# Optimization experiments

Hardware: AMD Instinct MI355X
Metric: run time of the kernel (lower is better)

Reference implementation:

```python
import jax, jax.numpy as jnp
import numpy as np

N_USERS = 100000
N_ITEMS = 100000
N = N_USERS + N_ITEMS
E = 3200000
TXT = 768
GREC = 16
D = 32            # embedding_dim (hardcoded 32 in the torch module)
LAYERS = 3        # len(weight_size)


def setup_inputs() -> dict:
    key = jax.random.key(0)
    ks = jax.random.split(key, 20)
    inp = {}
    inp["edge_row"] = jax.random.randint(ks[0], (E,), 0, N, dtype=jnp.int32)
    inp["edge_col"] = jax.random.randint(ks[1], (E,), 0, N, dtype=jnp.int32)
    # normalized adjacency values (positive, small)
    inp["adj_vals"] = jax.random.uniform(ks[2], (E,), dtype=jnp.float32) * 0.1
    inp["user_name_embs"] = jax.random.normal(ks[3], (N_USERS, TXT), dtype=jnp.float32)
    inp["sent_embs"] = jax.random.normal(ks[4], (N_ITEMS, TXT), dtype=jnp.float32)
    # learned params
    inp["user_emb"] = jax.random.normal(ks[5], (N_USERS, GREC), dtype=jnp.float32) * 0.1
    inp["item_emb"] = jax.random.normal(ks[6], (N_ITEMS, GREC), dtype=jnp.float32) * 0.1
    inp["ue_W1"] = jax.random.normal(ks[7], (TXT, 32), dtype=jnp.float32) * 0.05
    inp["ue_W2"] = jax.random.normal(ks[8], (32, GREC), dtype=jnp.float32) * 0.05
    inp["ie_W1"] = jax.random.normal(ks[9], (TXT, 32), dtype=jnp.float32) * 0.05
    inp["ie_W2"] = jax.random.normal(ks[10], (32, GREC), dtype=jnp.float32) * 0.05
    inp["gc_W"] = jax.random.normal(ks[11], (LAYERS, D, D), dtype=jnp.float32) * 0.1
    inp["gc_b"] = jnp.zeros((LAYERS, D), dtype=jnp.float32)
    inp["bi_W"] = jax.random.normal(ks[12], (LAYERS, D, D), dtype=jnp.float32) * 0.1
    inp["bi_b"] = jnp.zeros((LAYERS, D), dtype=jnp.float32)
    return inp


def _ngcf_forward(edge_row, edge_col, adj_vals, user_name_embs, sent_embs,
                  user_emb, item_emb, ue_W1, ue_W2, ie_W1, ie_W2,
                  gc_W, gc_b, bi_W, bi_b):
    # text encoders (Dropout is identity in eval mode)
    u_created = jax.nn.relu(user_name_embs @ ue_W1) @ ue_W2   # [Nu, 16]
    i_created = jax.nn.relu(sent_embs @ ie_W1) @ ie_W2         # [Ni, 16]
    agg_user = jnp.concatenate([user_emb, u_created], axis=1)  # [Nu, 32]
    agg_item = jnp.concatenate([item_emb, i_created], axis=1)  # [Ni, 32]
    ego = jnp.concatenate([agg_user, agg_item], axis=0)        # [N, 32]

    all_embeddings = [ego]
    for l in range(LAYERS):
        # sparse.mm(adj, ego): gather source rows, scale by edge value, scatter-add
        gathered = adj_vals[:, None] * ego[edge_col]           # [E, 32]
        side = jax.ops.segment_sum(gathered, edge_row, num_segments=N)  # [N, 32]
        sum_emb = jax.nn.leaky_relu(side @ gc_W[l] + gc_b[l])
        bi_emb = jax.nn.leaky_relu((ego * side) @ bi_W[l] + bi_b[l])
        ego = sum_emb + bi_emb                                 # dropout = identity (eval)
        norm = ego / jnp.maximum(
            jnp.linalg.norm(ego, axis=1, keepdims=True), 1e-12)
        all_embeddings.append(norm)
    return jnp.concatenate(all_embeddings, axis=1)             # [N, 32*(LAYERS+1)]


def reference(edge_row, edge_col, adj_vals, user_name_embs, sent_embs,
              user_emb, item_emb, ue_W1, ue_W2, ie_W1, ie_W2,
              gc_W, gc_b, bi_W, bi_b):
    all_e = _ngcf_forward(edge_row, edge_col, adj_vals, user_name_embs, sent_embs,
                          user_emb, item_emb, ue_W1, ue_W2, ie_W1, ie_W2,
                          gc_W, gc_b, bi_W, bi_b)
    u_g = all_e[:N_USERS]
    i_g = all_e[N_USERS:]
    return (u_g, i_g)
```

## Files before the change

### kernel.cpp

```cpp
#include <hip/hip_runtime.h>
#include <cstdint>

#define NU 100000
#define NI 100000
#define NN 200000
#define NE 3200000
#define TXT 768
#define DD 32
#define NRANGE 8
#define ROWS_PER_RANGE (NN / NRANGE)
#define NBJ 313

typedef _Float16 f16x8 __attribute__((ext_vector_type(8)));
typedef _Float16 f16x4 __attribute__((ext_vector_type(4)));
typedef float    f32x4 __attribute__((ext_vector_type(4)));

__device__ __forceinline__ float lrelu(float x) { return x >= 0.f ? x : 0.01f * x; }

__global__ void copy_emb_kernel(const float* __restrict__ uemb,
                                const float* __restrict__ iemb,
                                _Float16* __restrict__ ego16,
                                float* __restrict__ outp)
{
    int idx = blockIdx.x * blockDim.x + threadIdx.x;
    if (idx >= NN * 4) return;
    int n = idx >> 2, q = idx & 3;
    float4 v;
    if (n < NU) v = ((const float4*)uemb)[(size_t)n * 4 + q];
    else        v = ((const float4*)iemb)[(size_t)(n - NU) * 4 + q];
    f16x4 h;
    h[0] = (_Float16)v.x; h[1] = (_Float16)v.y;
    h[2] = (_Float16)v.z; h[3] = (_Float16)v.w;
    *(f16x4*)(ego16 + (size_t)n * 32 + q * 4) = h;
    ((float4*)outp)[(size_t)n * 32 + q] = v;
}

__global__ __launch_bounds__(256) void pack_w1_kernel(const float* __restrict__ ueW1,
                                                      const float* __restrict__ ieW1,
                                                      _Float16* __restrict__ w1p)
{
    const int i    = blockIdx.x * 256 + threadIdx.x;
    const int side = blockIdx.y;
    const float* W1 = side ? ieW1 : ueW1;
    int j   = i & 7;
    int ln  = (i >> 3) & 63;
    int kbH = i >> 9;
    int kb  = kbH >> 1, H = kbH & 1;
    int k   = kb * 32 + (ln >> 4) * 8 + j;
    int c   = H * 16 + (ln & 15);
    w1p[side * 24576 + i] = (_Float16)W1[k * 32 + c];
}

__global__ __launch_bounds__(512, 8) void mlp_mfma_kernel(
    const float* __restrict__ Xu, const float* __restrict__ Xi,
    const _Float16* __restrict__ w1pack,
    const float* __restrict__ ueW2, const float* __restrict__ ieW2,
    _Float16* __restrict__ ego16,
    float* __restrict__ outp)
{
    __shared__ _Float16 hbuf[8][640];

    const int tid  = threadIdx.x;
    const int lane = tid & 63;
    const int wv   = tid >> 6;

    const bool isU = blockIdx.x < 512;
    const float* X  = isU ? Xu : Xi;
    const _Float16* w1p = w1pack + (isU ? 0 : 24576);
    const float* W2 = isU ? ueW2 : ieW2;
    const int node_base = isU ? 0 : NU;
    const int bj = isU ? blockIdx.x : blockIdx.x - 512;

    f16x8 bw2;
    #pragma unroll
    for (int j = 0; j < 8; ++j)
        bw2[j] = (_Float16)W2[((lane >> 4) * 8 + j) * 16 + (lane & 15)];

    _Float16* hb = &hbuf[wv][0];
    const int gw = bj * 8 + wv;
    const int t0 = (int)(((long)gw * 6250) >> 12);
    const int t1 = (int)(((long)(gw + 1) * 6250) >> 12);

    for (int tile = t0; tile < t1; ++tile) {
        const float* xp = X + (size_t)(tile * 16 + (lane & 15)) * TXT + (lane >> 4) * 8;
        f32x4 c0 = {0.f, 0.f, 0.f, 0.f};
        f32x4 c1 = {0.f, 0.f, 0.f, 0.f};

        #pragma unroll 4
        for (int kb = 0; kb < 24; ++kb) {
            float4 xa = *(const float4*)(xp + kb * 32);
            float4 xb = *(const float4*)(xp + kb * 32 + 4);
            f16x8 b0 = *(const f16x8*)&w1p[(kb * 2 + 0) * 512 + lane * 8];
            f16x8 b1 = *(const f16x8*)&w1p[(kb * 2 + 1) * 512 + lane * 8];
            f16x8 a;
            a[0] = (_Float16)xa.x; a[1] = (_Float16)xa.y;
            a[2] = (_Float16)xa.z; a[3] = (_Float16)xa.w;
            a[4] = (_Float16)xb.x; a[5] = (_Float16)xb.y;
            a[6] = (_Float16)xb.z; a[7] = (_Float16)xb.w;
            c0 = __builtin_amdgcn_mfma_f32_16x16x32_f16(a, b0, c0, 0, 0, 0);
            c1 = __builtin_amdgcn_mfma_f32_16x16x32_f16(a, b1, c1, 0, 0, 0);
        }

        #pragma unroll
        for (int j = 0; j < 4; ++j) {
            int r = (lane >> 4) * 4 + j;
            hb[r * 40 + (lane & 15)]      = (_Float16)fmaxf(c0[j], 0.f);
            hb[r * 40 + (lane & 15) + 16] = (_Float16)fmaxf(c1[j], 0.f);
        }
        const _Float16* ap = &hb[(lane & 15) * 40 + (lane >> 4) * 8];
        f16x4 lo = *(const f16x4*)ap;
        f16x4 hi = *(const f16x4*)(ap + 4);
        f16x8 a2;
        a2[0] = lo[0]; a2[1] = lo[1]; a2[2] = lo[2]; a2[3] = lo[3];
        a2[4] = hi[0]; a2[5] = hi[1]; a2[6] = hi[2]; a2[7] = hi[3];

        f32x4 c2 = {0.f, 0.f, 0.f, 0.f};
        c2 = __builtin_amdgcn_mfma_f32_16x16x32_f16(a2, bw2, c2, 0, 0, 0);

        const int rbase = node_base + tile * 16 + (lane >> 4) * 4;
        const int j2 = lane & 15;
        #pragma unroll
        for (int j = 0; j < 4; ++j) {
            float v = c2[j];
            ego16[(size_t)(rbase + j) * 32  + 16 + j2] = (_Float16)v;
            outp [(size_t)(rbase + j) * 128 + 16 + j2] = v;
        }
    }
}

__global__ __launch_bounds__(256) void count_ranged_kernel(const int* __restrict__ erow,
                                                           int* __restrict__ cnt)
{
    const int rlo = (blockIdx.x & 7) * ROWS_PER_RANGE;
    const int rhi = rlo + ROWS_PER_RANGE;
    const int bj  = blockIdx.x >> 3;
    const int4* e4 = (const int4*)erow;
    for (int c = bj * 256 + threadIdx.x; c < NE / 4; c += NBJ * 256) {
        int4 v = e4[c];
        if (v.x >= rlo && v.x < rhi) atomicAdd(&cnt[v.x], 1);
        if (v.y >= rlo && v.y < rhi) atomicAdd(&cnt[v.y], 1);
        if (v.z >= rlo && v.z < rhi) atomicAdd(&cnt[v.z], 1);
        if (v.w >= rlo && v.w < rhi) atomicAdd(&cnt[v.w], 1);
    }
}

__global__ __launch_bounds__(256) void scan_blk_kernel(const int* __restrict__ cnt,
                                                       int* __restrict__ rp,
                                                       int* __restrict__ bsum)
{
    __shared__ int ts[256];
    const int tid = threadIdx.x;
    const int base = blockIdx.x * 1024 + tid * 4;
    int v0 = (base + 0 < NN) ? cnt[base + 0] : 0;
    int v1 = (base + 1 < NN) ? cnt[base + 1] : 0;
    int v2 = (base + 2 < NN) ? cnt[base + 2] : 0;
    int v3 = (base + 3 < NN) ? cnt[base + 3] : 0;
    int s = v0 + v1 + v2 + v3;
    ts[tid] = s;
    __syncthreads();
    for (int off = 1; off < 256; off <<= 1) {
        int t = (tid >= off) ? ts[tid - off] : 0;
        __syncthreads();
        ts[tid] += t;
        __syncthreads();
    }
    int excl = ts[tid] - s;
    if (base + 0 < NN) rp[base + 0] = excl;
    if (base + 1 < NN) rp[base + 1] = excl + v0;
    if (base + 2 < NN) rp[base + 2] = excl + v0 + v1;
    if (base + 3 < NN) rp[base + 3] = excl + v0 + v1 + v2;
    if (tid == 255) bsum[blockIdx.x] = ts[255];
}

__global__ __launch_bounds__(256) void scan_bsum_kernel(int* __restrict__ bsum, int nblk)
{
    __shared__ int ts[256];
    const int tid = threadIdx.x;
    int v = (tid < nblk) ? bsum[tid] : 0;
    ts[tid] = v;
    __syncthreads();
    for (int off = 1; off < 256; off <<= 1) {
        int t = (tid >= off) ? ts[tid - off] : 0;
        __syncthreads();
        ts[tid] += t;
        __syncthreads();
    }
    if (tid < nblk) bsum[tid] = ts[tid] - v;
}

__global__ __launch_bounds__(256) void add_off_kernel(int* __restrict__ rp,
                                                      const int* __restrict__ bsum,
                                                      int* __restrict__ cur)
{
    int i = blockIdx.x * 256 + threadIdx.x;
    if (i < NN) {
        int v = rp[i] + bsum[i >> 10];
        rp[i] = v;
        cur[i] = v;
    }
    if (i == 0) rp[NN] = NE;
}

__global__ __launch_bounds__(256) void fill_ranged_kernel(const int* __restrict__ erow,
                                                          const int* __restrict__ ecol,
                                                          const float* __restrict__ eval,
                                                          int* __restrict__ cur,
                                                          uint2* __restrict__ recs)
{
    const int rlo = (blockIdx.x & 7) * ROWS_PER_RANGE;
    const int rhi = rlo + ROWS_PER_RANGE;
    const int bj  = blockIdx.x >> 3;
    const int4* e4 = (const int4*)erow;
    for (int c = bj * 256 + threadIdx.x; c < NE / 4; c += NBJ * 256) {
        int4 v = e4[c];
        int base = c * 4;
        if (v.x >= rlo && v.x < rhi) {
            int pos = atomicAdd(&cur[v.x], 1);
            recs[pos] = make_uint2((unsigned)ecol[base+0] | ((unsigned)(v.x & 63) << 18),
                                   __float_as_uint(eval[base+0]));
        }
        if (v.y >= rlo && v.y < rhi) {
            int pos = atomicAdd(&cur[v.y], 1);
            recs[pos] = make_uint2((unsigned)ecol[base+1] | ((unsigned)(v.y & 63) << 18),
                                   __float_as_uint(eval[base+1]));
        }
        if (v.z >= rlo && v.z < rhi) {
            int pos = atomicAdd(&cur[v.z], 1);
            recs[pos] = make_uint2((unsigned)ecol[base+2] | ((unsigned)(v.z & 63) << 18),
                                   __float_as_uint(eval[base+2]));
        }
        if (v.w >= rlo && v.w < rhi) {
            int pos = atomicAdd(&cur[v.w], 1);
            recs[pos] = make_uint2((unsigned)ecol[base+3] | ((unsigned)(v.w & 63) << 18),
                                   __float_as_uint(eval[base+3]));
        }
    }
}

__global__ __launch_bounds__(256) void pull_update_v2(
    const int* __restrict__ rp, const uint2* __restrict__ recs,
    const _Float16* __restrict__ egoIn, _Float16* __restrict__ egoOut,
    float* __restrict__ outp,
    const float* __restrict__ gcW, const float* __restrict__ gcb,
    const float* __restrict__ biW, const float* __restrict__ bib, int l)
{
    __shared__ float acc[64][33];
    __shared__ float Wg[32][36];
    __shared__ float Wb[32][36];
    __shared__ float bgs[32], bbs[32];

    const int tid = threadIdx.x;
    for (int i = tid; i < 64 * 33; i += 256) ((float*)acc)[i] = 0.f;
    for (int i = tid; i < 1024; i += 256) {
        Wg[i >> 5][i & 31] = gcW[l * 1024 + i];
        Wb[i >> 5][i & 31] = biW[l * 1024 + i];
    }
    if (tid < 32) { bgs[tid] = gcb[l * 32 + tid]; bbs[tid] = bib[l * 32 + tid]; }

    const int r0 = blockIdx.x * 64;
    const int eBeg = rp[r0], eEnd = rp[r0 + 64];
    __syncthreads();

    const int cnt = eEnd - eBeg;
    const int s   = tid >> 3;
    const int q   = tid & 7;
    const int L   = (cnt + 31) >> 5;
    const int e0  = eBeg + s * L;
    const int e1  = min(e0 + L, eEnd);

    float4 a4 = make_float4(0.f, 0.f, 0.f, 0.f);
    int curRl = -1;
    for (int e = e0; e < e1; ++e) {
        uint2 rec = recs[e];
        int col = rec.x & 0x3FFFF;
        int rl  = rec.x >> 18;
        float a = __uint_as_float(rec.y);
        f16x4 v = *(const f16x4*)(egoIn + (size_t)col * 32 + q * 4);
        if (rl != curRl) {
            if (curRl >= 0) {
                atomicAdd(&acc[curRl][q * 4 + 0], a4.x);
                atomicAdd(&acc[curRl][q * 4 + 1], a4.y);
                atomicAdd(&acc[curRl][q * 4 + 2], a4.z);
                atomicAdd(&acc[curRl][q * 4 + 3], a4.w);
            }
            a4 = make_float4(0.f, 0.f, 0.f, 0.f);
            curRl = rl;
        }
        a4.x += a * (float)v[0];
        a4.y += a * (float)v[1];
        a4.z += a * (float)v[2];
        a4.w += a * (float)v[3];
    }
    if (curRl >= 0) {
        atomicAdd(&acc[curRl][q * 4 + 0], a4.x);
        atomicAdd(&acc[curRl][q * 4 + 1], a4.y);
        atomicAdd(&acc[curRl][q * 4 + 2], a4.z);
        atomicAdd(&acc[curRl][q * 4 + 3], a4.w);
    }
    __syncthreads();

    const int r    = tid >> 2;
    const int c    = tid & 3;
    const int node = r0 + r;
    const int j0   = c * 8;

    const _Float16* er = egoIn + (size_t)node * 32;
    f16x8 ev0 = *(const f16x8*)er;
    f16x8 ev1 = *(const f16x8*)(er + 8);
    f16x8 ev2 = *(const f16x8*)(er + 16);
    f16x8 ev3 = *(const f16x8*)(er + 24);

    float A[8], B[8];
    #pragma unroll
    for (int jj = 0; jj < 8; ++jj) { A[jj] = bgs[j0 + jj]; B[jj] = bbs[j0 + jj]; }

    #pragma unroll
    for (int kq = 0; kq < 4; ++kq) {
        #pragma unroll
        for (int kk = 0; kk < 8; ++kk) {
            const int k = kq * 8 + kk;
            float sk = acc[r][k];
            float evk = (kq == 0) ? (float)ev0[kk] : (kq == 1) ? (float)ev1[kk]
                      : (kq == 2) ? (float)ev2[kk] : (float)ev3[kk];
            float ek = sk * evk;
            f32x4 g0 = *(const f32x4*)&Wg[k][j0];
            f32x4 g1 = *(const f32x4*)&Wg[k][j0 + 4];
            f32x4 b0 = *(const f32x4*)&Wb[k][j0];
            f32x4 b1 = *(const f32x4*)&Wb[k][j0 + 4];
            A[0] += sk * g0[0]; A[1] += sk * g0[1]; A[2] += sk * g0[2]; A[3] += sk * g0[3];
            A[4] += sk * g1[0]; A[5] += sk * g1[1]; A[6] += sk * g1[2]; A[7] += sk * g1[3];
            B[0] += ek * b0[0]; B[1] += ek * b0[1]; B[2] += ek * b0[2]; B[3] += ek * b0[3];
            B[4] += ek * b1[0]; B[5] += ek * b1[1]; B[6] += ek * b1[2]; B[7] += ek * b1[3];
        }
    }

    float v[8];
    float ss = 0.f;
    #pragma unroll
    for (int jj = 0; jj < 8; ++jj) {
        float x = lrelu(A[jj]) + lrelu(B[jj]);
        v[jj] = x;
        ss += x * x;
    }
    ss += __shfl_xor(ss, 1, 64);
    ss += __shfl_xor(ss, 2, 64);
    float inv = 1.0f / fmaxf(sqrtf(ss), 1e-12f);

    f16x8 h;
    #pragma unroll
    for (int jj = 0; jj < 8; ++jj) h[jj] = (_Float16)v[jj];
    *(f16x8*)(egoOut + (size_t)node * 32 + j0) = h;

    float* op = outp + (size_t)node * 128 + (size_t)(l + 1) * 32 + j0;
    float4 o0 = make_float4(v[0] * inv, v[1] * inv, v[2] * inv, v[3] * inv);
    float4 o1 = make_float4(v[4] * inv, v[5] * inv, v[6] * inv, v[7] * inv);
    *(float4*)op       = o0;
    *(float4*)(op + 4) = o1;
}

extern "C" void kernel_launch(void* const* d_in, const int* in_sizes, int n_in,
                              void* d_out, int out_size, void* d_ws, size_t ws_size,
                              hipStream_t stream)
{
    const int*   erow = (const int*)d_in[0];
    const int*   ecol = (const int*)d_in[1];
    const float* evalp = (const float*)d_in[2];
    const float* une  = (const float*)d_in[3];
    const float* se   = (const float*)d_in[4];
    const float* uemb = (const float*)d_in[5];
    const float* iemb = (const float*)d_in[6];
    const float* ueW1 = (const float*)d_in[7];
    const float* ueW2 = (const float*)d_in[8];
    const float* ieW1 = (const float*)d_in[9];
    const float* ieW2 = (const float*)d_in[10];
    const float* gcW  = (const float*)d_in[11];
    const float* gcb  = (const float*)d_in[12];
    const float* biW  = (const float*)d_in[13];
    const float* bib  = (const float*)d_in[14];
    float* outp = (float*)d_out;

    _Float16* egoA16 = (_Float16*)d_ws;
    _Float16* egoB16 = egoA16 + (size_t)NN * 32;
    uint2* recs = (uint2*)(egoB16 + (size_t)NN * 32);
    int*   cnt  = (int*)(recs + (size_t)NE);
    int*   rp   = cnt + NN;
    int*   cur  = rp + NN + 1;
    int*   bsum = cur + NN;
    _Float16* w1pack = (_Float16*)(bsum + 256);

    const size_t need = (size_t)((char*)(w1pack + 49152) - (char*)d_ws);
    if (ws_size < need) return;

    pack_w1_kernel<<<dim3(96, 2), 256, 0, stream>>>(ueW1, ieW1, w1pack);
    copy_emb_kernel<<<(NN * 4 + 255) / 256, 256, 0, stream>>>(uemb, iemb, egoA16, outp);
    mlp_mfma_kernel<<<1024, 512, 0, stream>>>(une, se, w1pack, ueW2, ieW2,
                                              egoA16, outp);

    const int NBLK = (NN + 1023) / 1024;
    hipMemsetAsync(cnt, 0, (size_t)NN * sizeof(int), stream);
    count_ranged_kernel<<<NRANGE * NBJ, 256, 0, stream>>>(erow, cnt);
    scan_blk_kernel<<<NBLK, 256, 0, stream>>>(cnt, rp, bsum);
    scan_bsum_kernel<<<1, 256, 0, stream>>>(bsum, NBLK);
    add_off_kernel<<<(NN + 255) / 256, 256, 0, stream>>>(rp, bsum, cur);
    fill_ranged_kernel<<<NRANGE * NBJ, 256, 0, stream>>>(erow, ecol, evalp, cur, recs);

    const _Float16* egoIn = egoA16;
    _Float16* egoOut = egoB16;
    for (int l = 0; l < 3; ++l) {
        pull_update_v2<<<NN / 64, 256, 0, stream>>>(rp, recs, egoIn, egoOut, outp,
                                                    gcW, gcb, biW, bib, l);
        const _Float16* t = egoOut; egoOut = (_Float16*)egoIn; egoIn = t;
    }
}
```

Measured before the change: 790.2 us.

## Merge prep kernels, stage MLP inputs via async LDS loads, unroll gather loop

Folds edge counting, embedding copy and W1 packing into one prep kernel to cut launch count and let the independent work run concurrently. The text-encoder MFMA kernel now double-buffers input tiles in shared memory through direct global-to-LDS loads with a swizzled layout, instead of per-lane strided global loads. Its occupancy hint drops to 4 blocks and it uses 64KB of LDS. The pull kernel issues four gathers at a time so more memory loads are in flight. Risks include lower occupancy and fragile hand-written waitcnt ordering.

Result: faster. 739.2 us (-6.5%).

```diff
diff --git a/kernel.cpp b/kernel.cpp
--- a/kernel.cpp
+++ b/kernel.cpp
@@ -15,50 +15,69 @@
 typedef _Float16 f16x4 __attribute__((ext_vector_type(4)));
 typedef float    f32x4 __attribute__((ext_vector_type(4)));
 
+typedef __attribute__((address_space(1))) const unsigned int guint;
+typedef __attribute__((address_space(3))) unsigned int luint;
+
 __device__ __forceinline__ float lrelu(float x) { return x >= 0.f ? x : 0.01f * x; }
 
-__global__ void copy_emb_kernel(const float* __restrict__ uemb,
-                                const float* __restrict__ iemb,
-                                _Float16* __restrict__ ego16,
-                                float* __restrict__ outp)
-{
-    int idx = blockIdx.x * blockDim.x + threadIdx.x;
-    if (idx >= NN * 4) return;
-    int n = idx >> 2, q = idx & 3;
-    float4 v;
-    if (n < NU) v = ((const float4*)uemb)[(size_t)n * 4 + q];
-    else        v = ((const float4*)iemb)[(size_t)(n - NU) * 4 + q];
-    f16x4 h;
-    h[0] = (_Float16)v.x; h[1] = (_Float16)v.y;
-    h[2] = (_Float16)v.z; h[3] = (_Float16)v.w;
-    *(f16x4*)(ego16 + (size_t)n * 32 + q * 4) = h;
-    ((float4*)outp)[(size_t)n * 32 + q] = v;
-}
-
-__global__ __launch_bounds__(256) void pack_w1_kernel(const float* __restrict__ ueW1,
-                                                      const float* __restrict__ ieW1,
-                                                      _Float16* __restrict__ w1p)
-{
-    const int i    = blockIdx.x * 256 + threadIdx.x;
-    const int side = blockIdx.y;
-    const float* W1 = side ? ieW1 : ueW1;
-    int j   = i & 7;
-    int ln  = (i >> 3) & 63;
-    int kbH = i >> 9;
-    int kb  = kbH >> 1, H = kbH & 1;
-    int k   = kb * 32 + (ln >> 4) * 8 + j;
-    int c   = H * 16 + (ln & 15);
-    w1p[side * 24576 + i] = (_Float16)W1[k * 32 + c];
-}
-
-__global__ __launch_bounds__(512, 8) void mlp_mfma_kernel(
+__global__ __launch_bounds__(256) void prep_kernel(
+    const int* __restrict__ erow,
+    const float* __restrict__ uemb, const float* __restrict__ iemb,
+    const float* __restrict__ ueW1, const float* __restrict__ ieW1,
+    int* __restrict__ cnt,
+    _Float16* __restrict__ ego16, float* __restrict__ outp,
+    _Float16* __restrict__ w1p)
+{
+    const int b = blockIdx.x;
+    const int tid = threadIdx.x;
+
+    if (b < 2504) {
+        const int rlo = (b & 7) * ROWS_PER_RANGE;
+        const int rhi = rlo + ROWS_PER_RANGE;
+        const int bj  = b >> 3;
+        const int4* e4 = (const int4*)erow;
+        for (int c = bj * 256 + tid; c < NE / 4; c += NBJ * 256) {
+            int4 v = e4[c];
+            if (v.x >= rlo && v.x < rhi) atomicAdd(&cnt[v.x], 1);
+            if (v.y >= rlo && v.y < rhi) atomicAdd(&cnt[v.y], 1);
+            if (v.z >= rlo && v.z < rhi) atomicAdd(&cnt[v.z], 1);
+            if (v.w >= rlo && v.w < rhi) atomicAdd(&cnt[v.w], 1);
+        }
+    } else if (b < 2504 + 3125) {
+        int idx = (b - 2504) * 256 + tid;
+        if (idx >= NN * 4) return;
+        int n = idx >> 2, q = idx & 3;
+        float4 v;
+        if (n < NU) v = ((const float4*)uemb)[(size_t)n * 4 + q];
+        else        v = ((const float4*)iemb)[(size_t)(n - NU) * 4 + q];
+        f16x4 h;
+        h[0] = (_Float16)v.x; h[1] = (_Float16)v.y;
+        h[2] = (_Float16)v.z; h[3] = (_Float16)v.w;
+        *(f16x4*)(ego16 + (size_t)n * 32 + q * 4) = h;
+        ((float4*)outp)[(size_t)n * 32 + q] = v;
+    } else {
+        int i = (b - 5629) * 256 + tid;
+        int side = (i >= 24576);
+        int ii = i - side * 24576;
+        const float* W1 = side ? ieW1 : ueW1;
+        int j   = ii & 7;
+        int ln  = (ii >> 3) & 63;
+        int kbH = ii >> 9;
+        int kb  = kbH >> 1, H = kbH & 1;
+        int k   = kb * 32 + (ln >> 4) * 8 + j;
+        int c   = H * 16 + (ln & 15);
+        w1p[i] = (_Float16)W1[k * 32 + c];
+    }
+}
+
+__global__ __launch_bounds__(512, 4) void mlp_mfma_v3(
     const float* __restrict__ Xu, const float* __restrict__ Xi,
     const _Float16* __restrict__ w1pack,
     const float* __restrict__ ueW2, const float* __restrict__ ieW2,
     _Float16* __restrict__ ego16,
     float* __restrict__ outp)
 {
-    __shared__ _Float16 hbuf[8][640];
+    __shared__ float sbuf[16384];
 
     const int tid  = threadIdx.x;
     const int lane = tid & 63;
@@ -71,36 +90,71 @@
     const int node_base = isU ? 0 : NU;
     const int bj = isU ? blockIdx.x : blockIdx.x - 512;
 
+    const int r16 = lane & 15;
+    const int cg  = lane >> 4;
+    const int rx  = r16 & 7;
+
     f16x8 bw2;
     #pragma unroll
     for (int j = 0; j < 8; ++j)
         bw2[j] = (_Float16)W2[((lane >> 4) * 8 + j) * 16 + (lane & 15)];
 
-    _Float16* hb = &hbuf[wv][0];
+    float* wbuf = &sbuf[wv * 2048];
+
+#define STAGE(bufidx, cc) do {                                                   \
+        _Pragma("unroll")                                                        \
+        for (int i_ = 0; i_ < 4; ++i_) {                                         \
+            int r_ = i_ * 4 + (lane >> 4);                                       \
+            int s_ = (lane & 15) ^ (r_ & 7);                                     \
+            const float* g_ = xtile + (size_t)r_ * TXT + (cc) * 64 + s_ * 4;     \
+            __builtin_amdgcn_global_load_lds((guint*)g_,                         \
+                (luint*)(wbuf + (bufidx) * 1024 + i_ * 256), 16, 0, 0);          \
+        }                                                                        \
+    } while (0)
+
     const int gw = bj * 8 + wv;
     const int t0 = (int)(((long)gw * 6250) >> 12);
     const int t1 = (int)(((long)(gw + 1) * 6250) >> 12);
 
     for (int tile = t0; tile < t1; ++tile) {
-        const float* xp = X + (size_t)(tile * 16 + (lane & 15)) * TXT + (lane >> 4) * 8;
+        const float* xtile = X + (size_t)tile * 16 * TXT;
+        asm volatile("s_waitcnt lgkmcnt(0)" ::: "memory");
+        STAGE(0, 0);
+        STAGE(1, 1);
+
         f32x4 c0 = {0.f, 0.f, 0.f, 0.f};
         f32x4 c1 = {0.f, 0.f, 0.f, 0.f};
 
-        #pragma unroll 4
-        for (int kb = 0; kb < 24; ++kb) {
-            float4 xa = *(const float4*)(xp + kb * 32);
-            float4 xb = *(const float4*)(xp + kb * 32 + 4);
-            f16x8 b0 = *(const f16x8*)&w1p[(kb * 2 + 0) * 512 + lane * 8];
-            f16x8 b1 = *(const f16x8*)&w1p[(kb * 2 + 1) * 512 + lane * 8];
-            f16x8 a;
-            a[0] = (_Float16)xa.x; a[1] = (_Float16)xa.y;
-            a[2] = (_Float16)xa.z; a[3] = (_Float16)xa.w;
-            a[4] = (_Float16)xb.x; a[5] = (_Float16)xb.y;
-            a[6] = (_Float16)xb.z; a[7] = (_Float16)xb.w;
-            c0 = __builtin_amdgcn_mfma_f32_16x16x32_f16(a, b0, c0, 0, 0, 0);
-            c1 = __builtin_amdgcn_mfma_f32_16x16x32_f16(a, b1, c1, 0, 0, 0);
-        }
-
+        #pragma unroll
+        for (int c = 0; c < 12; ++c) {
+            if (c == 11) asm volatile("s_waitcnt vmcnt(0)" ::: "memory");
+            else         asm volatile("s_waitcnt vmcnt(4)" ::: "memory");
+
+            #pragma unroll
+            for (int k2 = 0; k2 < 2; ++k2) {
+                const int kb = c * 2 + k2;
+                f16x8 b0 = *(const f16x8*)&w1p[(kb * 2 + 0) * 512 + lane * 8];
+                f16x8 b1 = *(const f16x8*)&w1p[(kb * 2 + 1) * 512 + lane * 8];
+                const int s0 = k2 * 8 + cg * 2;
+                const float* p0 = wbuf + (c & 1) * 1024 + (r16 * 16 + (s0 ^ rx)) * 4;
+                const float* p1 = wbuf + (c & 1) * 1024 + (r16 * 16 + ((s0 + 1) ^ rx)) * 4;
+                f32x4 xa = *(const f32x4*)p0;
+                f32x4 xb = *(const f32x4*)p1;
+                f16x8 a;
+                a[0] = (_Float16)xa[0]; a[1] = (_Float16)xa[1];
+                a[2] = (_Float16)xa[2]; a[3] = (_Float16)xa[3];
+                a[4] = (_Float16)xb[0]; a[5] = (_Float16)xb[1];
+                a[6] = (_Float16)xb[2]; a[7] = (_Float16)xb[3];
+                c0 = __builtin_amdgcn_mfma_f32_16x16x32_f16(a, b0, c0, 0, 0, 0);
+                c1 = __builtin_amdgcn_mfma_f32_16x16x32_f16(a, b1, c1, 0, 0, 0);
+            }
+            if (c < 10) {
+                asm volatile("s_waitcnt lgkmcnt(0)" ::: "memory");
+                STAGE(c & 1, c + 2);
+            }
+        }
+
+        _Float16* hb = (_Float16*)wbuf;
         #pragma unroll
         for (int j = 0; j < 4; ++j) {
             int r = (lane >> 4) * 4 + j;
@@ -126,22 +180,7 @@
             outp [(size_t)(rbase + j) * 128 + 16 + j2] = v;
         }
     }
-}
-
-__global__ __launch_bounds__(256) void count_ranged_kernel(const int* __restrict__ erow,
-                                                           int* __restrict__ cnt)
-{
-    const int rlo = (blockIdx.x & 7) * ROWS_PER_RANGE;
-    const int rhi = rlo + ROWS_PER_RANGE;
-    const int bj  = blockIdx.x >> 3;
-    const int4* e4 = (const int4*)erow;
-    for (int c = bj * 256 + threadIdx.x; c < NE / 4; c += NBJ * 256) {
-        int4 v = e4[c];
-        if (v.x >= rlo && v.x < rhi) atomicAdd(&cnt[v.x], 1);
-        if (v.y >= rlo && v.y < rhi) atomicAdd(&cnt[v.y], 1);
-        if (v.z >= rlo && v.z < rhi) atomicAdd(&cnt[v.z], 1);
-        if (v.w >= rlo && v.w < rhi) atomicAdd(&cnt[v.w], 1);
-    }
+#undef STAGE
 }
 
 __global__ __launch_bounds__(256) void scan_blk_kernel(const int* __restrict__ cnt,
@@ -270,12 +309,10 @@
 
     float4 a4 = make_float4(0.f, 0.f, 0.f, 0.f);
     int curRl = -1;
-    for (int e = e0; e < e1; ++e) {
-        uint2 rec = recs[e];
-        int col = rec.x & 0x3FFFF;
-        int rl  = rec.x >> 18;
-        float a = __uint_as_float(rec.y);
-        f16x4 v = *(const f16x4*)(egoIn + (size_t)col * 32 + q * 4);
+
+    auto PROC = [&](uint2 rr, f16x4 vv) {
+        int rl = rr.x >> 18;
+        float a = __uint_as_float(rr.y);
         if (rl != curRl) {
             if (curRl >= 0) {
                 atomicAdd(&acc[curRl][q * 4 + 0], a4.x);
@@ -286,10 +323,26 @@
             a4 = make_float4(0.f, 0.f, 0.f, 0.f);
             curRl = rl;
         }
-        a4.x += a * (float)v[0];
-        a4.y += a * (float)v[1];
-        a4.z += a * (float)v[2];
-        a4.w += a * (float)v[3];
+        a4.x += a * (float)vv[0];
+        a4.y += a * (float)vv[1];
+        a4.z += a * (float)vv[2];
+        a4.w += a * (float)vv[3];
+    };
+
+    int e = e0;
+    for (; e + 4 <= e1; e += 4) {
+        uint2 r0r = recs[e],     r1r = recs[e + 1];
+        uint2 r2r = recs[e + 2], r3r = recs[e + 3];
+        f16x4 v0 = *(const f16x4*)(egoIn + (size_t)(r0r.x & 0x3FFFF) * 32 + q * 4);
+        f16x4 v1 = *(const f16x4*)(egoIn + (size_t)(r1r.x & 0x3FFFF) * 32 + q * 4);
+        f16x4 v2 = *(const f16x4*)(egoIn + (size_t)(r2r.x & 0x3FFFF) * 32 + q * 4);
+        f16x4 v3 = *(const f16x4*)(egoIn + (size_t)(r3r.x & 0x3FFFF) * 32 + q * 4);
+        PROC(r0r, v0); PROC(r1r, v1); PROC(r2r, v2); PROC(r3r, v3);
+    }
+    for (; e < e1; ++e) {
+        uint2 rr = recs[e];
+        f16x4 vv = *(const f16x4*)(egoIn + (size_t)(rr.x & 0x3FFFF) * 32 + q * 4);
+        PROC(rr, vv);
     }
     if (curRl >= 0) {
         atomicAdd(&acc[curRl][q * 4 + 0], a4.x);
@@ -391,14 +444,14 @@
     const size_t need = (size_t)((char*)(w1pack + 49152) - (char*)d_ws);
     if (ws_size < need) return;
 
-    pack_w1_kernel<<<dim3(96, 2), 256, 0, stream>>>(ueW1, ieW1, w1pack);
-    copy_emb_kernel<<<(NN * 4 + 255) / 256, 256, 0, stream>>>(uemb, iemb, egoA16, outp);
-    mlp_mfma_kernel<<<1024, 512, 0, stream>>>(une, se, w1pack, ueW2, ieW2,
-                                              egoA16, outp);
+    hipMemsetAsync(cnt, 0, (size_t)NN * sizeof(int), stream);
+    prep_kernel<<<5821, 256, 0, stream>>>(erow, uemb, iemb, ueW1, ieW1,
+                                          cnt, egoA16, outp, w1pack);
+
+    mlp_mfma_v3<<<1024, 512, 0, stream>>>(une, se, w1pack, ueW2, ieW2,
+                                          egoA16, outp);
 
     const int NBLK = (NN + 1023) / 1024;
-    hipMemsetAsync(cnt, 0, (size_t)NN * sizeof(int), stream);
-    count_ranged_kernel<<<NRANGE * NBJ, 256, 0, stream>>>(erow, cnt);
     scan_blk_kernel<<<NBLK, 256, 0, stream>>>(cnt, rp, bsum);
     scan_bsum_kernel<<<1, 256, 0, stream>>>(bsum, NBLK);
     add_off_kernel<<<(NN + 255) / 256, 256, 0, stream>>>(rp, bsum, cur);
```
